# Kernel optimization log

Hardware: AMD Instinct MI355X
Metric: run time of the kernel (lower is better)

## Reference

```python
import jax, jax.numpy as jnp
import numpy as np

D_MODEL = 2048
N_HEADS = 16
HEAD_DIM = D_MODEL // N_HEADS
ROPE_THETA = 10000.0
B, S = 2, 2048
MAX_POS = 8192


def _rope(x, position_ids):
    # x: [b, h, s, hd]; position_ids: [b, s] int
    half = HEAD_DIM // 2
    inv_freq = 1.0 / (ROPE_THETA ** (jnp.arange(0, HEAD_DIM, 2, dtype=jnp.float32) / HEAD_DIM))  # [half]
    ang = position_ids[..., None].astype(jnp.float32) * inv_freq  # [b, s, half]
    cos = jnp.concatenate([jnp.cos(ang), jnp.cos(ang)], axis=-1)[:, None]  # [b, 1, s, hd]
    sin = jnp.concatenate([jnp.sin(ang), jnp.sin(ang)], axis=-1)[:, None]
    x1, x2 = x[..., :half], x[..., half:]
    rot = jnp.concatenate([-x2, x1], axis=-1)  # rotate_half
    return x * cos + rot * sin


def setup_inputs() -> dict:
    key = jax.random.key(0)
    ks = jax.random.split(key, 6)
    wscale = 1.0 / np.sqrt(D_MODEL)
    x_sparse = jax.random.normal(ks[0], (B, S, D_MODEL), dtype=jnp.float32)
    Wq = jax.random.normal(ks[1], (D_MODEL, D_MODEL), dtype=jnp.float32) * wscale
    Wk = jax.random.normal(ks[2], (D_MODEL, D_MODEL), dtype=jnp.float32) * wscale
    Wv = jax.random.normal(ks[3], (D_MODEL, D_MODEL), dtype=jnp.float32) * wscale
    Wo = jax.random.normal(ks[4], (D_MODEL, D_MODEL), dtype=jnp.float32) * wscale
    position_ids = jnp.sort(jax.random.randint(ks[5], (B, S), 0, MAX_POS), axis=-1).astype(jnp.int64)
    return {"x_sparse": x_sparse, "Wq": Wq, "Wk": Wk, "Wv": Wv, "Wo": Wo, "position_ids": position_ids}


def reference(x_sparse, Wq, Wk, Wv, Wo, position_ids):
    b, s, d = x_sparse.shape

    def heads(W):
        return (x_sparse @ W).reshape(b, s, N_HEADS, HEAD_DIM).transpose(0, 2, 1, 3)  # [b,h,s,hd]

    q = _rope(heads(Wq), position_ids)
    k = _rope(heads(Wk), position_ids)
    v = heads(Wv)

    scores = jnp.einsum('bhqd,bhkd->bhqk', q, k) / np.float32(np.sqrt(HEAD_DIM))
    # dynamic position-based causal mask: pos_i >= pos_j, broadcast over heads
    mask = position_ids[:, None, :, None] >= position_ids[:, None, None, :]  # [b,1,s,s]
    scores = jnp.where(mask, scores, jnp.float32(-1e30))
    attn = jax.nn.softmax(scores, axis=-1)
    out = jnp.einsum('bhqk,bhkd->bhqd', attn, v)  # [b,h,s,hd]
    out = out.transpose(0, 2, 1, 3).reshape(b, s, d)
    return out @ Wo
```

## Files before the change

kernel.cpp:

```cpp
#include <hip/hip_runtime.h>
#include <stdint.h>


typedef unsigned short u16;
typedef unsigned int u32;
typedef __attribute__((ext_vector_type(8))) short bf16x8;
typedef __attribute__((ext_vector_type(4))) float f32x4;

#define SEQ 2048
#define DM 2048
#define NH 16
#define HD 128
#define SM_SCALE 0.08838834764831845f
#define K2LOG 0.12751743f

__device__ __forceinline__ u16 f2bf(float f) {
  union { float f; uint32_t u; } v; v.f = f;
  uint32_t u = v.u + 0x7fffu + ((v.u >> 16) & 1u);
  return (u16)(u >> 16);
}
__device__ __forceinline__ float bf2f(u16 h) {
  union { uint32_t u; float f; } v; v.u = ((uint32_t)h) << 16; return v.f;
}
__device__ __forceinline__ u32 pack2(float a, float b) {
  return (u32)f2bf(a) | ((u32)f2bf(b) << 16);
}
__device__ __forceinline__ u32 pack2_trunc(float a, float b) {
  union { float f; u32 u; } x, y; x.f = a; y.f = b;
  return (x.u >> 16) | (y.u & 0xFFFF0000u);
}

__device__ __forceinline__ void gl2lds16(const void* g, void* l) {
  __builtin_amdgcn_global_load_lds(
      (const __attribute__((address_space(1))) uint32_t*)g,
      (__attribute__((address_space(3))) uint32_t*)l, 16, 0, 0);
}

__global__ __launch_bounds__(256) void cvt_x(const float* __restrict__ x, u16* __restrict__ xb) {
  int i = blockIdx.x * 256 + threadIdx.x;
  float4 v = ((const float4*)x)[i];
  uint2 r;
  r.x = pack2(v.x, v.y);
  r.y = pack2(v.z, v.w);
  ((uint2*)xb)[i] = r;
}

__global__ __launch_bounds__(256) void wtrans(const float* __restrict__ w0, const float* __restrict__ w1,
                                              const float* __restrict__ w2, const float* __restrict__ w3,
                                              u16* __restrict__ dst) {
  const float* W = blockIdx.z == 0 ? w0 : blockIdx.z == 1 ? w1 : blockIdx.z == 2 ? w2 : w3;
  u16* D = dst + (size_t)blockIdx.z * DM * DM;
  int k0 = blockIdx.x * 32, n0 = blockIdx.y * 32;
  __shared__ u16 t[32][33];
  int tx = threadIdx.x, ty = threadIdx.y;
#pragma unroll
  for (int i = 0; i < 32; i += 8)
    t[ty + i][tx] = f2bf(W[(size_t)(k0 + ty + i) * DM + n0 + tx]);
  __syncthreads();
#pragma unroll
  for (int i = 0; i < 32; i += 8)
    D[(size_t)(n0 + ty + i) * DM + k0 + tx] = t[tx][ty + i];
}

__device__ __forceinline__ void gemm_core(const u16* __restrict__ A, const u16* __restrict__ Bt,
                                          int m0, int n0, u16* As, u16* Bs, f32x4 acc[4][4]) {
  int tid = threadIdx.x, lane = tid & 63;
  int l15 = lane & 15, quad = lane >> 4;
  int wave = tid >> 6;
  int wm = (wave >> 1) * 64, wn = (wave & 1) * 64;
  for (int k0 = 0; k0 < DM; k0 += 64) {
#pragma unroll
    for (int i = 0; i < 4; ++i) {
      int s = i * 256 + tid;
      int row = s >> 3, c = (s & 7) ^ (row & 7);
      gl2lds16(&A[(size_t)(m0 + row) * DM + k0 + c * 8], &As[(s & ~63) * 8]);
      gl2lds16(&Bt[(size_t)(n0 + row) * DM + k0 + c * 8], &Bs[(s & ~63) * 8]);
    }
    __syncthreads();
#pragma unroll
    for (int kk = 0; kk < 2; ++kk) {
      bf16x8 af[4], bfr[4];
#pragma unroll
      for (int mt = 0; mt < 4; ++mt) {
        int row = wm + mt * 16 + l15;
        int c = (kk * 4 + quad) ^ (row & 7);
        af[mt] = *(const bf16x8*)&As[row * 64 + c * 8];
      }
#pragma unroll
      for (int nt = 0; nt < 4; ++nt) {
        int row = wn + nt * 16 + l15;
        int c = (kk * 4 + quad) ^ (row & 7);
        bfr[nt] = *(const bf16x8*)&Bs[row * 64 + c * 8];
      }
#pragma unroll
      for (int mt = 0; mt < 4; ++mt)
#pragma unroll
        for (int nt = 0; nt < 4; ++nt)
          acc[mt][nt] = __builtin_amdgcn_mfma_f32_16x16x32_bf16(af[mt], bfr[nt], acc[mt][nt], 0, 0, 0);
    }
    __syncthreads();
  }
}

__global__ __launch_bounds__(256) void qkv_gemm(const u16* __restrict__ X, const u16* __restrict__ Wt,
                                                u16* __restrict__ Qo, u16* __restrict__ Ko,
                                                u16* __restrict__ Vto) {
  __shared__ u16 As[128 * 64];
  __shared__ u16 Bs[128 * 64];
  const u16* Bt = Wt + (size_t)blockIdx.z * DM * DM;
  int n0 = blockIdx.x * 128, m0 = blockIdx.y * 128;
  f32x4 acc[4][4] = {};
  gemm_core(X, Bt, m0, n0, As, Bs, acc);
  int lane = threadIdx.x & 63, wave = threadIdx.x >> 6;
  int l15 = lane & 15, quad = lane >> 4;
  int wm = (wave >> 1) * 64, wn = (wave & 1) * 64;
  if (blockIdx.z == 2) {
    int h = n0 >> 7;
#pragma unroll
    for (int mt = 0; mt < 4; ++mt)
#pragma unroll
      for (int nt = 0; nt < 4; ++nt) {
        int tok = m0 + wm + mt * 16 + quad * 4;
        int d = wn + nt * 16 + l15;
        int b = tok >> 11, sx = tok & (SEQ - 1);
        u16* dp = &Vto[((size_t)(b * NH + h) * HD + d) * SEQ + sx];
        *(u32*)&dp[0] = pack2(acc[mt][nt][0], acc[mt][nt][1]);
        *(u32*)&dp[2] = pack2(acc[mt][nt][2], acc[mt][nt][3]);
      }
  } else {
    u16* C = blockIdx.z == 0 ? Qo : Ko;
#pragma unroll
    for (int mt = 0; mt < 4; ++mt)
#pragma unroll
      for (int nt = 0; nt < 4; ++nt)
#pragma unroll
        for (int r = 0; r < 4; ++r)
          C[(size_t)(m0 + wm + mt * 16 + quad * 4 + r) * DM + n0 + wn + nt * 16 + l15]
              = f2bf(acc[mt][nt][r]);
  }
}

__global__ __launch_bounds__(256) void proj_gemm(const u16* __restrict__ A, const u16* __restrict__ Wt,
                                                 float* __restrict__ C) {
  __shared__ u16 As[128 * 64];
  __shared__ u16 Bs[128 * 64];
  int n0 = blockIdx.x * 128, m0 = blockIdx.y * 128;
  f32x4 acc[4][4] = {};
  gemm_core(A, Wt, m0, n0, As, Bs, acc);
  int lane = threadIdx.x & 63, wave = threadIdx.x >> 6;
  int l15 = lane & 15, quad = lane >> 4;
  int wm = (wave >> 1) * 64, wn = (wave & 1) * 64;
#pragma unroll
  for (int mt = 0; mt < 4; ++mt)
#pragma unroll
    for (int nt = 0; nt < 4; ++nt)
#pragma unroll
      for (int r = 0; r < 4; ++r)
        C[(size_t)(m0 + wm + mt * 16 + quad * 4 + r) * DM + n0 + wn + nt * 16 + l15] = acc[mt][nt][r];
}

__global__ __launch_bounds__(256) void rope_k(u16* __restrict__ Q, u16* __restrict__ K,
                                              const int* __restrict__ pos) {
  uint32_t idx = blockIdx.x * 256 + threadIdx.x;
  int i = idx & 63;
  int h = (idx >> 6) & 15;
  int s = (idx >> 10) & 2047;
  int b = idx >> 21;
  u16* P = (blockIdx.y == 0) ? Q : K;
  int p = pos[b * SEQ + s];
  float inv_rev = exp2f(fmaf((float)i, -0.20762051f, -2.6514961f));
  float pf = (float)p;
  float hi = pf * inv_rev;
  float err = fmaf(pf, inv_rev, -hi);
  float r = (hi - truncf(hi)) + err;
  float ang = r * 6.2831853f;
  float sn = __sinf(ang), cs = __cosf(ang);
  size_t base = ((size_t)(b * SEQ + s)) * DM + h * HD;
  float x1 = bf2f(P[base + i]), x2 = bf2f(P[base + 64 + i]);
  P[base + i] = f2bf(x1 * cs - x2 * sn);
  P[base + 64 + i] = f2bf(x2 * cs + x1 * sn);
}

__global__ __launch_bounds__(256, 2) void attn_k(const u16* __restrict__ Q, const u16* __restrict__ K,
                                                 const u16* __restrict__ Vt, const int* __restrict__ pos,
                                                 u16* __restrict__ AO) {
  __shared__ u16 Ks[2][64 * 128];
  __shared__ u16 Vs[2][128 * 64];
  int tid = threadIdx.x, lane = tid & 63, wave = tid >> 6;
  int bx = blockIdx.x;
  int bh = bx & 31;
  int g4 = bx >> 5;
  int g = (bh & 1) ? (15 - g4) : g4;
  int b = bh >> 4, h = bh & 15;
  int stripe = 4 * g + wave;
  int l15 = lane & 15, quad = lane >> 4;
  const int* posb = pos + b * SEQ;
  int qbase = stripe * 32;
  const u16* Kg = &K[(size_t)(b * SEQ) * DM + h * HD];
  const u16* Vg = &Vt[(size_t)(b * NH + h) * HD * SEQ];

  bf16x8 qf[2][4];
#pragma unroll
  for (int qi = 0; qi < 2; ++qi)
#pragma unroll
    for (int kk = 0; kk < 4; ++kk)
      qf[qi][kk] = *(const bf16x8*)&Q[(size_t)(b * SEQ + qbase + qi * 16 + l15) * DM
                                      + h * HD + kk * 32 + quad * 8];

  auto ub = [&](int v) {
    int c = 0;
#pragma unroll
    for (int st = 1024; st; st >>= 1)
      if (posb[c + st - 1] <= v) c += st;
    if (c == 2047 && posb[2047] <= v) c = 2048;
    return c;
  };
  int cnt[2];
  cnt[0] = ub(posb[qbase + l15]);
  cnt[1] = ub(posb[qbase + 16 + l15]);
  int cnt_min = ub(posb[qbase]);
  int cnt_max = ub(posb[qbase + 31]);
  int ntile = (cnt_max + 63) >> 6;
  int cnt_blk = ub(posb[(4 * g + 3) * 32 + 31]);
  int ntile_blk = (cnt_blk + 63) >> 6;

  auto STAGE = [&](int j0, int bufi) {
#pragma unroll
    for (int i = 0; i < 4; ++i) {
      int s = i * 256 + tid;
      int rk = s >> 4, ck = (s & 15) ^ (rk & 15);
      gl2lds16(&Kg[(size_t)(j0 + rk) * DM + ck * 8], &Ks[bufi][(s & ~63) * 8]);
      int rv = s >> 3, cv = (s & 7) ^ (rv & 7);
      gl2lds16(&Vg[(size_t)rv * SEQ + j0 + cv * 8], &Vs[bufi][(s & ~63) * 8]);
    }
  };

  STAGE(0, 0);
  __syncthreads();

  float m_i[2] = {-1.0e30f, -1.0e30f}, l_i[2] = {0.0f, 0.0f};
  f32x4 oacc[2][8] = {};

  int base0 = l15 + ((quad & 1) << 5);
  bool hi_sel = (quad >> 1) != 0;

  for (int j = 0; j < ntile_blk; ++j) {
    int cur = j & 1;
    if (j + 1 < ntile_blk) STAGE((j + 1) * 64, cur ^ 1);

    if (j < ntile) {
      int j0 = j * 64;

      f32x4 sacc[2][4] = {};
#pragma unroll
      for (int kt = 0; kt < 4; ++kt) {
        bf16x8 kfa[4];
#pragma unroll
        for (int kk = 0; kk < 4; ++kk) {
          int cs = (kk * 4 + quad) ^ l15;
          kfa[kk] = *(const bf16x8*)&Ks[cur][((kt * 16 + l15) * 16 + cs) * 8];
        }
#pragma unroll
        for (int qi = 0; qi < 2; ++qi)
#pragma unroll
          for (int kk = 0; kk < 4; ++kk)
            sacc[qi][kt] = __builtin_amdgcn_mfma_f32_16x16x32_bf16(kfa[kk], qf[qi][kk], sacc[qi][kt], 0, 0, 0);
      }

      bool need_mask = (j0 + 64 > cnt_min);
      u32 pb[2][4][2];
#pragma unroll
      for (int qi = 0; qi < 2; ++qi) {
        if (need_mask) {
          int rel = cnt[qi] - j0;
#pragma unroll
          for (int kt = 0; kt < 4; ++kt)
#pragma unroll
            for (int r = 0; r < 4; ++r)
              if (kt * 16 + quad * 4 + r >= rel) sacc[qi][kt][r] = -1.0e30f;
        }
        float mx = fmaxf(fmaxf(sacc[qi][0][0], sacc[qi][0][1]), fmaxf(sacc[qi][0][2], sacc[qi][0][3]));
#pragma unroll
        for (int kt = 1; kt < 4; ++kt)
          mx = fmaxf(mx, fmaxf(fmaxf(sacc[qi][kt][0], sacc[qi][kt][1]),
                               fmaxf(sacc[qi][kt][2], sacc[qi][kt][3])));
        mx = fmaxf(mx, __shfl_xor(mx, 16));
        mx = fmaxf(mx, __shfl_xor(mx, 32));
        float mold = m_i[qi];
        float mn = fmaxf(mold, mx);
        if (__any(mn > mold)) {
          float al = exp2f((mold - mn) * K2LOG);
          l_i[qi] *= al;
#pragma unroll
          for (int dt = 0; dt < 8; ++dt) oacc[qi][dt] *= al;
          m_i[qi] = mn;
        }
        float nc = -m_i[qi] * K2LOG;
        float rs = 0.0f;
#pragma unroll
        for (int kt = 0; kt < 4; ++kt) {
          float p0 = exp2f(fmaf(sacc[qi][kt][0], K2LOG, nc));
          float p1 = exp2f(fmaf(sacc[qi][kt][1], K2LOG, nc));
          float p2 = exp2f(fmaf(sacc[qi][kt][2], K2LOG, nc));
          float p3 = exp2f(fmaf(sacc[qi][kt][3], K2LOG, nc));
          rs += (p0 + p1) + (p2 + p3);
          pb[qi][kt][0] = pack2_trunc(p0, p1);
          pb[qi][kt][1] = pack2_trunc(p2, p3);
        }
        rs += __shfl_xor(rs, 16);
        rs += __shfl_xor(rs, 32);
        l_i[qi] += rs;
      }

#pragma unroll
      for (int kk2 = 0; kk2 < 2; ++kk2) {
        bf16x8 vf[8];
#pragma unroll
        for (int dt = 0; dt < 8; ++dt) {
          int cs = (kk2 * 4 + quad) ^ (l15 & 7);
          vf[dt] = *(const bf16x8*)&Vs[cur][((dt * 16 + l15) * 8 + cs) * 8];
        }
#pragma unroll
        for (int qi = 0; qi < 2; ++qi) {
          u32 w[4];
#pragma unroll
          for (int wd = 0; wd < 4; ++wd) {
            int src = base0 + ((wd >> 1) << 4);
            u32 va = __shfl(pb[qi][kk2 * 2 + 0][wd & 1], src);
            u32 vb = __shfl(pb[qi][kk2 * 2 + 1][wd & 1], src);
            w[wd] = hi_sel ? vb : va;
          }
          union { bf16x8 v; u32 u[4]; } pt;
          pt.u[0] = w[0]; pt.u[1] = w[1]; pt.u[2] = w[2]; pt.u[3] = w[3];
#pragma unroll
          for (int dt = 0; dt < 8; ++dt)
            oacc[qi][dt] = __builtin_amdgcn_mfma_f32_16x16x32_bf16(vf[dt], pt.v, oacc[qi][dt], 0, 0, 0);
        }
      }
    }
    __syncthreads();
  }

#pragma unroll
  for (int qi = 0; qi < 2; ++qi) {
    float inv = 1.0f / l_i[qi];
    u16* aop = &AO[(size_t)(b * SEQ + qbase + qi * 16 + l15) * DM + h * HD];
#pragma unroll
    for (int dt = 0; dt < 8; ++dt) {
      int col = dt * 16 + quad * 4;
      *(u32*)&aop[col]     = pack2(oacc[qi][dt][0] * inv, oacc[qi][dt][1] * inv);
      *(u32*)&aop[col + 2] = pack2(oacc[qi][dt][2] * inv, oacc[qi][dt][3] * inv);
    }
  }
}

extern "C" void kernel_launch(void* const* d_in, const int* in_sizes, int n_in,
                              void* d_out, int out_size, void* d_ws, size_t ws_size,
                              hipStream_t stream) {
  const float* x  = (const float*)d_in[0];
  const float* Wq = (const float*)d_in[1];
  const float* Wk = (const float*)d_in[2];
  const float* Wv = (const float*)d_in[3];
  const float* Wo = (const float*)d_in[4];
  const int*  pos = (const int*)d_in[5];
  float* out = (float*)d_out;

  u16* ws  = (u16*)d_ws;
  u16* xb  = ws;
  u16* wt  = xb  + (size_t)4096 * 2048;
  u16* qb  = wt  + (size_t)4 * 2048 * 2048;
  u16* kb  = qb  + (size_t)4096 * 2048;
  u16* vtb = kb  + (size_t)4096 * 2048;
  u16* aob = vtb + (size_t)4096 * 2048;

  cvt_x<<<8192, 256, 0, stream>>>(x, xb);
  wtrans<<<dim3(64, 64, 4), dim3(32, 8), 0, stream>>>(Wq, Wk, Wv, Wo, wt);
  qkv_gemm<<<dim3(16, 32, 3), 256, 0, stream>>>(xb, wt, qb, kb, vtb);
  rope_k<<<dim3(16384, 2), 256, 0, stream>>>(qb, kb, pos);
  attn_k<<<dim3(512), 256, 0, stream>>>(qb, kb, vtb, pos, aob);
  proj_gemm<<<dim3(16, 32), 256, 0, stream>>>(aob, wt + (size_t)3 * 2048 * 2048, out);
}
```

Measured before the change: 425.5 us.

## Rewrite QKV GEMM as 256x256 tile, 8-wave, double-buffered kernel

Replaces the 128x128 four-wave QKV GEMM with a 256x256 tile computed by eight waves. It double-buffers LDS with direct global-to-LDS loads, interleaves fragment loads with MFMA bursts under raised wave priority, and swizzles block order for L2 locality. The larger tile raises arithmetic intensity and overlaps global fetch with compute. In exchange it uses 128 KB of LDS and many registers per block, which limits occupancy, and it adds many barriers per K step.

```diff
diff --git a/kernel.cpp b/kernel.cpp
--- a/kernel.cpp
+++ b/kernel.cpp
@@ -102,41 +102,129 @@
   }
 }
 
-__global__ __launch_bounds__(256) void qkv_gemm(const u16* __restrict__ X, const u16* __restrict__ Wt,
-                                                u16* __restrict__ Qo, u16* __restrict__ Ko,
-                                                u16* __restrict__ Vto) {
-  __shared__ u16 As[128 * 64];
-  __shared__ u16 Bs[128 * 64];
-  const u16* Bt = Wt + (size_t)blockIdx.z * DM * DM;
-  int n0 = blockIdx.x * 128, m0 = blockIdx.y * 128;
-  f32x4 acc[4][4] = {};
-  gemm_core(X, Bt, m0, n0, As, Bs, acc);
-  int lane = threadIdx.x & 63, wave = threadIdx.x >> 6;
+__global__ __launch_bounds__(512, 2) void qkv_gemm8(const u16* __restrict__ X, const u16* __restrict__ Wt,
+                                                    u16* __restrict__ Qo, u16* __restrict__ Ko,
+                                                    u16* __restrict__ Vto) {
+  __shared__ u16 As[2][256 * 64];
+  __shared__ u16 Bs[2][256 * 64];
+  int tid = threadIdx.x, lane = tid & 63;
   int l15 = lane & 15, quad = lane >> 4;
-  int wm = (wave >> 1) * 64, wn = (wave & 1) * 64;
-  if (blockIdx.z == 2) {
-    int h = n0 >> 7;
-#pragma unroll
-    for (int mt = 0; mt < 4; ++mt)
-#pragma unroll
-      for (int nt = 0; nt < 4; ++nt) {
-        int tok = m0 + wm + mt * 16 + quad * 4;
-        int d = wn + nt * 16 + l15;
+  int w = tid >> 6, wm = w >> 2, wn = w & 3;
+  int bid = blockIdx.x;
+  int swz = (bid & 7) * 48 + (bid >> 3);
+  int by = swz / 24, bx = swz % 24;
+  int z = bx >> 3;
+  int n0 = (bx & 7) * 256;
+  int m0 = by * 256;
+  const u16* Bt = Wt + (size_t)z * DM * DM;
+
+  auto SH = [&](const u16* S, int rb, int kt, u16* L, int h) {
+#pragma unroll
+    for (int i = 0; i < 2; ++i) {
+      int s = i * 512 + tid;
+      int r = s >> 3, c = (s & 7) ^ (r & 7);
+      gl2lds16(&S[(size_t)(rb + h * 128 + r) * DM + kt + c * 8],
+               &L[h * 128 * 64 + (s & ~63) * 8]);
+    }
+  };
+
+  f32x4 acc[8][4] = {};
+  bf16x8 a0[4], a1[4], bb[4][2];
+
+  auto LDA = [&](bf16x8* dst, int mg, int kk, const u16* Ac) {
+#pragma unroll
+    for (int mi = 0; mi < 4; ++mi) {
+      int row = wm * 128 + (mg * 4 + mi) * 16 + l15;
+      dst[mi] = *(const bf16x8*)&Ac[row * 64 + (((kk * 4 + quad) ^ (row & 7)) * 8)];
+    }
+  };
+  auto LDB = [&](int kk, const u16* Bc) {
+#pragma unroll
+    for (int ni = 0; ni < 4; ++ni) {
+      int row = wn * 64 + ni * 16 + l15;
+      bb[ni][kk] = *(const bf16x8*)&Bc[row * 64 + (((kk * 4 + quad) ^ (row & 7)) * 8)];
+    }
+  };
+  auto MM = [&](bf16x8* af, int mg, int kk) {
+    __builtin_amdgcn_s_setprio(1);
+#pragma unroll
+    for (int mi = 0; mi < 4; ++mi)
+#pragma unroll
+      for (int ni = 0; ni < 4; ++ni)
+        acc[mg * 4 + mi][ni] =
+            __builtin_amdgcn_mfma_f32_16x16x32_bf16(af[mi], bb[ni][kk], acc[mg * 4 + mi][ni], 0, 0, 0);
+    __builtin_amdgcn_s_setprio(0);
+  };
+
+  SH(X, m0, 0, (u16*)As[0], 0); SH(X, m0, 0, (u16*)As[0], 1);
+  SH(Bt, n0, 0, (u16*)Bs[0], 0); SH(Bt, n0, 0, (u16*)Bs[0], 1);
+  asm volatile("s_waitcnt vmcnt(0)" ::: "memory");
+  __builtin_amdgcn_s_barrier();
+
+  for (int t = 0; t < 32; ++t) {
+    const u16* Ac = As[t & 1];
+    const u16* Bc = Bs[t & 1];
+    LDA(a0, 0, 0, Ac);
+    LDB(0, Bc);
+    if (t < 31) {
+      int kt1 = (t + 1) * 64;
+      u16* An = (u16*)As[(t & 1) ^ 1];
+      u16* Bn = (u16*)Bs[(t & 1) ^ 1];
+      SH(X, m0, kt1, An, 0); SH(X, m0, kt1, An, 1);
+      SH(Bt, n0, kt1, Bn, 0); SH(Bt, n0, kt1, Bn, 1);
+    }
+    asm volatile("" ::: "memory");
+    __builtin_amdgcn_s_barrier();
+    asm volatile("s_waitcnt lgkmcnt(0)" ::: "memory");
+    MM(a0, 0, 0);
+    __builtin_amdgcn_s_barrier();
+    LDA(a1, 1, 0, Ac);
+    asm volatile("" ::: "memory");
+    __builtin_amdgcn_s_barrier();
+    asm volatile("s_waitcnt lgkmcnt(0)" ::: "memory");
+    MM(a1, 1, 0);
+    __builtin_amdgcn_s_barrier();
+    LDA(a0, 0, 1, Ac);
+    LDB(1, Bc);
+    asm volatile("" ::: "memory");
+    __builtin_amdgcn_s_barrier();
+    asm volatile("s_waitcnt lgkmcnt(0)" ::: "memory");
+    MM(a0, 0, 1);
+    __builtin_amdgcn_s_barrier();
+    LDA(a1, 1, 1, Ac);
+    asm volatile("" ::: "memory");
+    __builtin_amdgcn_s_barrier();
+    asm volatile("s_waitcnt lgkmcnt(0)" ::: "memory");
+    MM(a1, 1, 1);
+    asm volatile("s_waitcnt vmcnt(0)" ::: "memory");
+    __builtin_amdgcn_s_barrier();
+  }
+
+  int wmbase = m0 + wm * 128;
+  int wnbase = n0 + wn * 64;
+  if (z == 2) {
+#pragma unroll
+    for (int mi = 0; mi < 8; ++mi)
+#pragma unroll
+      for (int ni = 0; ni < 4; ++ni) {
+        int tok = wmbase + mi * 16 + quad * 4;
+        int d = wnbase + ni * 16 + l15;
+        int h = d >> 7, dh = d & 127;
         int b = tok >> 11, sx = tok & (SEQ - 1);
-        u16* dp = &Vto[((size_t)(b * NH + h) * HD + d) * SEQ + sx];
-        *(u32*)&dp[0] = pack2(acc[mt][nt][0], acc[mt][nt][1]);
-        *(u32*)&dp[2] = pack2(acc[mt][nt][2], acc[mt][nt][3]);
+        u16* dp = &Vto[((size_t)(b * NH + h) * HD + dh) * SEQ + sx];
+        *(u32*)&dp[0] = pack2(acc[mi][ni][0], acc[mi][ni][1]);
+        *(u32*)&dp[2] = pack2(acc[mi][ni][2], acc[mi][ni][3]);
       }
   } else {
-    u16* C = blockIdx.z == 0 ? Qo : Ko;
-#pragma unroll
-    for (int mt = 0; mt < 4; ++mt)
-#pragma unroll
-      for (int nt = 0; nt < 4; ++nt)
+    u16* C = (z == 0) ? Qo : Ko;
+#pragma unroll
+    for (int mi = 0; mi < 8; ++mi)
+#pragma unroll
+      for (int ni = 0; ni < 4; ++ni)
 #pragma unroll
         for (int r = 0; r < 4; ++r)
-          C[(size_t)(m0 + wm + mt * 16 + quad * 4 + r) * DM + n0 + wn + nt * 16 + l15]
-              = f2bf(acc[mt][nt][r]);
+          C[(size_t)(wmbase + mi * 16 + quad * 4 + r) * DM + wnbase + ni * 16 + l15]
+              = f2bf(acc[mi][ni][r]);
   }
 }
 
@@ -250,7 +338,6 @@
 
     if (j < ntile) {
       int j0 = j * 64;
-
       f32x4 sacc[2][4] = {};
 #pragma unroll
       for (int kt = 0; kt < 4; ++kt) {
@@ -322,16 +409,16 @@
         }
 #pragma unroll
         for (int qi = 0; qi < 2; ++qi) {
-          u32 w[4];
+          u32 wv[4];
 #pragma unroll
           for (int wd = 0; wd < 4; ++wd) {
             int src = base0 + ((wd >> 1) << 4);
             u32 va = __shfl(pb[qi][kk2 * 2 + 0][wd & 1], src);
             u32 vb = __shfl(pb[qi][kk2 * 2 + 1][wd & 1], src);
-            w[wd] = hi_sel ? vb : va;
+            wv[wd] = hi_sel ? vb : va;
           }
           union { bf16x8 v; u32 u[4]; } pt;
-          pt.u[0] = w[0]; pt.u[1] = w[1]; pt.u[2] = w[2]; pt.u[3] = w[3];
+          pt.u[0] = wv[0]; pt.u[1] = wv[1]; pt.u[2] = wv[2]; pt.u[3] = wv[3];
 #pragma unroll
           for (int dt = 0; dt < 8; ++dt)
             oacc[qi][dt] = __builtin_amdgcn_mfma_f32_16x16x32_bf16(vf[dt], pt.v, oacc[qi][dt], 0, 0, 0);
@@ -375,7 +462,7 @@
 
   cvt_x<<<8192, 256, 0, stream>>>(x, xb);
   wtrans<<<dim3(64, 64, 4), dim3(32, 8), 0, stream>>>(Wq, Wk, Wv, Wo, wt);
-  qkv_gemm<<<dim3(16, 32, 3), 256, 0, stream>>>(xb, wt, qb, kb, vtb);
+  qkv_gemm8<<<dim3(384), 512, 0, stream>>>(xb, wt, qb, kb, vtb);
   rope_k<<<dim3(16384, 2), 256, 0, stream>>>(qb, kb, pos);
   attn_k<<<dim3(512), 256, 0, stream>>>(qb, kb, vtb, pos, aob);
   proj_gemm<<<dim3(16, 32), 256, 0, stream>>>(aob, wt + (size_t)3 * 2048 * 2048, out);
```

New measurement: 446.5 us. +4.9%, slower.

## Fuse RoPE into QKV GEMM epilogue via shared-memory tile and rebalance attention grid

Applied to the files above, without the earlier changes.

Removes the standalone RoPE kernel and applies rotary embedding in the QKV GEMM epilogue. The output tile is staged through swizzled shared memory so each thread can read both rotation partners, which are 64 columns apart within a head. This drops a full read-modify-write pass over Q and K and one kernel launch. It also changes the attention block-to-stripe mapping so that early and late causal stripes are paired differently, aiming for better load balance. The cost is extra LDS traffic and a sync in the GEMM epilogue, plus sin/cos work there.

```diff
diff --git a/kernel.cpp b/kernel.cpp
--- a/kernel.cpp
+++ b/kernel.cpp
@@ -103,14 +103,14 @@
 }
 
 __global__ __launch_bounds__(256) void qkv_gemm(const u16* __restrict__ X, const u16* __restrict__ Wt,
+                                                const int* __restrict__ pos,
                                                 u16* __restrict__ Qo, u16* __restrict__ Ko,
                                                 u16* __restrict__ Vto) {
-  __shared__ u16 As[128 * 64];
-  __shared__ u16 Bs[128 * 64];
+  __shared__ u16 smem[2][128 * 64];
   const u16* Bt = Wt + (size_t)blockIdx.z * DM * DM;
   int n0 = blockIdx.x * 128, m0 = blockIdx.y * 128;
   f32x4 acc[4][4] = {};
-  gemm_core(X, Bt, m0, n0, As, Bs, acc);
+  gemm_core(X, Bt, m0, n0, smem[0], smem[1], acc);
   int lane = threadIdx.x & 63, wave = threadIdx.x >> 6;
   int l15 = lane & 15, quad = lane >> 4;
   int wm = (wave >> 1) * 64, wn = (wave & 1) * 64;
@@ -128,15 +128,50 @@
         *(u32*)&dp[2] = pack2(acc[mt][nt][2], acc[mt][nt][3]);
       }
   } else {
+    u16* tile = smem[0];
+#pragma unroll
+    for (int mt = 0; mt < 4; ++mt)
+#pragma unroll
+      for (int nt = 0; nt < 4; ++nt)
+#pragma unroll
+        for (int r = 0; r < 4; ++r) {
+          int row = wm + mt * 16 + quad * 4 + r;
+          int col = wn + nt * 16 + l15;
+          int cs = col ^ (((row >> 2) & 3) << 4);
+          tile[row * 128 + cs] = f2bf(acc[mt][nt][r]);
+        }
+    __syncthreads();
     u16* C = blockIdx.z == 0 ? Qo : Ko;
+    float invrev[4];
+#pragma unroll
+    for (int nt = 0; nt < 4; ++nt) {
+      int i = (nt * 16 + l15) & 63;
+      invrev[nt] = exp2f(fmaf((float)i, -0.20762051f, -2.6514961f));
+    }
+    bool second_half = (wn != 0);
 #pragma unroll
     for (int mt = 0; mt < 4; ++mt)
 #pragma unroll
-      for (int nt = 0; nt < 4; ++nt)
-#pragma unroll
-        for (int r = 0; r < 4; ++r)
-          C[(size_t)(m0 + wm + mt * 16 + quad * 4 + r) * DM + n0 + wn + nt * 16 + l15]
-              = f2bf(acc[mt][nt][r]);
+      for (int r = 0; r < 4; ++r) {
+        int row = wm + mt * 16 + quad * 4 + r;
+        int tok = m0 + row;
+        int b = tok >> 11, sx = tok & (SEQ - 1);
+        float pf = (float)pos[b * SEQ + sx];
+        int sw = ((row >> 2) & 3) << 4;
+#pragma unroll
+        for (int nt = 0; nt < 4; ++nt) {
+          int col = wn + nt * 16 + l15;
+          float hv = pf * invrev[nt];
+          float err = fmaf(pf, invrev[nt], -hv);
+          float fr = (hv - truncf(hv)) + err;
+          float ang = fr * 6.2831853f;
+          float sn = __sinf(ang), cs2 = __cosf(ang);
+          float own = bf2f(tile[row * 128 + (col ^ sw)]);
+          float par = bf2f(tile[row * 128 + ((col ^ 64) ^ sw)]);
+          float out = second_half ? fmaf(own, cs2, par * sn) : (own * cs2 - par * sn);
+          C[(size_t)tok * DM + n0 + col] = f2bf(out);
+        }
+      }
   }
 }
 
@@ -159,28 +194,6 @@
         C[(size_t)(m0 + wm + mt * 16 + quad * 4 + r) * DM + n0 + wn + nt * 16 + l15] = acc[mt][nt][r];
 }
 
-__global__ __launch_bounds__(256) void rope_k(u16* __restrict__ Q, u16* __restrict__ K,
-                                              const int* __restrict__ pos) {
-  uint32_t idx = blockIdx.x * 256 + threadIdx.x;
-  int i = idx & 63;
-  int h = (idx >> 6) & 15;
-  int s = (idx >> 10) & 2047;
-  int b = idx >> 21;
-  u16* P = (blockIdx.y == 0) ? Q : K;
-  int p = pos[b * SEQ + s];
-  float inv_rev = exp2f(fmaf((float)i, -0.20762051f, -2.6514961f));
-  float pf = (float)p;
-  float hi = pf * inv_rev;
-  float err = fmaf(pf, inv_rev, -hi);
-  float r = (hi - truncf(hi)) + err;
-  float ang = r * 6.2831853f;
-  float sn = __sinf(ang), cs = __cosf(ang);
-  size_t base = ((size_t)(b * SEQ + s)) * DM + h * HD;
-  float x1 = bf2f(P[base + i]), x2 = bf2f(P[base + 64 + i]);
-  P[base + i] = f2bf(x1 * cs - x2 * sn);
-  P[base + 64 + i] = f2bf(x2 * cs + x1 * sn);
-}
-
 __global__ __launch_bounds__(256, 2) void attn_k(const u16* __restrict__ Q, const u16* __restrict__ K,
                                                  const u16* __restrict__ Vt, const int* __restrict__ pos,
                                                  u16* __restrict__ AO) {
@@ -190,7 +203,7 @@
   int bx = blockIdx.x;
   int bh = bx & 31;
   int g4 = bx >> 5;
-  int g = (bh & 1) ? (15 - g4) : g4;
+  int g = (g4 < 8) ? g4 : (23 - g4);
   int b = bh >> 4, h = bh & 15;
   int stripe = 4 * g + wave;
   int l15 = lane & 15, quad = lane >> 4;
@@ -250,7 +263,6 @@
 
     if (j < ntile) {
       int j0 = j * 64;
-
       f32x4 sacc[2][4] = {};
 #pragma unroll
       for (int kt = 0; kt < 4; ++kt) {
@@ -322,16 +334,16 @@
         }
 #pragma unroll
         for (int qi = 0; qi < 2; ++qi) {
-          u32 w[4];
+          u32 wv[4];
 #pragma unroll
           for (int wd = 0; wd < 4; ++wd) {
             int src = base0 + ((wd >> 1) << 4);
             u32 va = __shfl(pb[qi][kk2 * 2 + 0][wd & 1], src);
             u32 vb = __shfl(pb[qi][kk2 * 2 + 1][wd & 1], src);
-            w[wd] = hi_sel ? vb : va;
+            wv[wd] = hi_sel ? vb : va;
           }
           union { bf16x8 v; u32 u[4]; } pt;
-          pt.u[0] = w[0]; pt.u[1] = w[1]; pt.u[2] = w[2]; pt.u[3] = w[3];
+          pt.u[0] = wv[0]; pt.u[1] = wv[1]; pt.u[2] = wv[2]; pt.u[3] = wv[3];
 #pragma unroll
           for (int dt = 0; dt < 8; ++dt)
             oacc[qi][dt] = __builtin_amdgcn_mfma_f32_16x16x32_bf16(vf[dt], pt.v, oacc[qi][dt], 0, 0, 0);
@@ -375,8 +387,7 @@
 
   cvt_x<<<8192, 256, 0, stream>>>(x, xb);
   wtrans<<<dim3(64, 64, 4), dim3(32, 8), 0, stream>>>(Wq, Wk, Wv, Wo, wt);
-  qkv_gemm<<<dim3(16, 32, 3), 256, 0, stream>>>(xb, wt, qb, kb, vtb);
-  rope_k<<<dim3(16384, 2), 256, 0, stream>>>(qb, kb, pos);
+  qkv_gemm<<<dim3(16, 32, 3), 256, 0, stream>>>(xb, wt, pos, qb, kb, vtb);
   attn_k<<<dim3(512), 256, 0, stream>>>(qb, kb, vtb, pos, aob);
   proj_gemm<<<dim3(16, 32), 256, 0, stream>>>(aob, wt + (size_t)3 * 2048 * 2048, out);
 }
```

Result: faster. 410.7 us (-3.5%).
